# Kernel tuning notes

Hardware: AMD Instinct MI355X
Metric: run time of the kernel (lower is better)

The kernel has to match this reference:

```python
import jax, jax.numpy as jnp
import numpy as np

B, S, E, H = 2, 2048, 1024, 16
HD = E // H


def setup_inputs() -> dict:
    key = jax.random.key(0)
    ks = jax.random.split(key, 5)
    scale = 1.0 / np.sqrt(E)
    return {
        "x": jax.random.normal(ks[0], (B, S, E), dtype=jnp.float32),
        "Wq": jax.random.normal(ks[1], (H, HD, E), dtype=jnp.float32) * scale,
        "Wk": jax.random.normal(ks[2], (H, HD, E), dtype=jnp.float32) * scale,
        "Wv": jax.random.normal(ks[3], (H, HD, E), dtype=jnp.float32) * scale,
        "Wo": jax.random.normal(ks[4], (E, E), dtype=jnp.float32) * scale,
    }


def reference(x, Wq, Wk, Wv, Wo):
    # Batched per-head projections: torch Linear y = x @ W.T, W: [head_dim, E]
    q = jnp.einsum("bse,hde->bshd", x, Wq)  # [B,S,H,HD]
    k = jnp.einsum("bse,hde->bshd", x, Wk)
    v = jnp.einsum("bse,hde->bshd", x, Wv)
    # Scaled dot-product attention; original scales by sqrt(head_dim)
    scores = jnp.einsum("bqhd,bkhd->bhqk", q, k) / jnp.sqrt(jnp.float32(HD))
    attn = jax.nn.softmax(scores, axis=-1)  # [B,H,S,S]
    out_h = jnp.einsum("bhqk,bkhd->bqhd", attn, v)  # [B,S,H,HD]
    out_cat = out_h.reshape(x.shape[0], x.shape[1], -1)  # concat heads -> [B,S,E]
    return out_cat @ Wo.T
```

## Files before the change

### kernel.cpp

```cpp
#include <hip/hip_runtime.h>
#include <hip/hip_bf16.h>

typedef unsigned short u16;
typedef unsigned int u32;
typedef __attribute__((ext_vector_type(4))) float f32x4;
typedef __attribute__((ext_vector_type(16))) float f32x16;
typedef __attribute__((ext_vector_type(8))) short short8;
typedef __attribute__((ext_vector_type(8))) unsigned short u16x8;
typedef __attribute__((ext_vector_type(4))) unsigned short u16x4;
typedef __attribute__((ext_vector_type(4))) unsigned int u32x4;

#define BATCH 2
#define SEQ   2048
#define EMB   1024
#define NH    16
#define HD    64

__device__ inline u16 f2bf(float f) {
    unsigned u = __builtin_bit_cast(unsigned, f);
    unsigned r = u + 0x7FFFu + ((u >> 16) & 1u);
    return (u16)(r >> 16);
}

__device__ inline float fexp2(float x) {
    float r;
    asm("v_exp_f32 %0, %1" : "=v"(r) : "v"(x));
    return r;
}

__device__ inline void gload16(const void* g, void* l) {
    __builtin_amdgcn_global_load_lds(
        (const __attribute__((address_space(1))) unsigned int*)g,
        (__attribute__((address_space(3))) unsigned int*)l, 16, 0, 0);
}

__device__ inline short8 mk8(u32 a, u32 b, u32 c, u32 d) {
    u32x4 t; t[0] = a; t[1] = b; t[2] = c; t[3] = d;
    return __builtin_bit_cast(short8, t);
}

#define PACK_ST(st, w0,w1,w2,w3,w4,w5,w6,w7)                                   \
  {                                                                            \
    asm("v_cvt_pk_bf16_f32 %0, %1, %2" : "=v"(w0) : "v"(st[0]),  "v"(st[1]));  \
    asm("v_cvt_pk_bf16_f32 %0, %1, %2" : "=v"(w1) : "v"(st[2]),  "v"(st[3]));  \
    asm("v_cvt_pk_bf16_f32 %0, %1, %2" : "=v"(w2) : "v"(st[4]),  "v"(st[5]));  \
    asm("v_cvt_pk_bf16_f32 %0, %1, %2" : "=v"(w3) : "v"(st[6]),  "v"(st[7]));  \
    asm("v_permlane32_swap_b32 %0, %1" : "+v"(w0), "+v"(w2));                  \
    asm("v_permlane32_swap_b32 %0, %1" : "+v"(w1), "+v"(w3));                  \
    asm("v_cvt_pk_bf16_f32 %0, %1, %2" : "=v"(w4) : "v"(st[8]),  "v"(st[9]));  \
    asm("v_cvt_pk_bf16_f32 %0, %1, %2" : "=v"(w5) : "v"(st[10]), "v"(st[11])); \
    asm("v_cvt_pk_bf16_f32 %0, %1, %2" : "=v"(w6) : "v"(st[12]), "v"(st[13])); \
    asm("v_cvt_pk_bf16_f32 %0, %1, %2" : "=v"(w7) : "v"(st[14]), "v"(st[15])); \
    asm("v_permlane32_swap_b32 %0, %1" : "+v"(w4), "+v"(w6));                  \
    asm("v_permlane32_swap_b32 %0, %1" : "+v"(w5), "+v"(w7));                  \
  }

__global__ __launch_bounds__(256) void convert_all(
    const float* __restrict__ x,
    const float* __restrict__ Wq, const float* __restrict__ Wk, const float* __restrict__ Wv,
    const float* __restrict__ Wo,
    u16* __restrict__ Xb, u16* __restrict__ Wqkv, u16* __restrict__ Wob)
{
    const int bid = blockIdx.x;
    const float* src;
    u16* dst;
    if (bid < 3584) {
        const long gidx = (long)bid * 2048 + (long)threadIdx.x * 8;
        if (gidx < 4194304L) {
            src = x + gidx; dst = Xb + gidx;
        } else {
            const long r = gidx - 4194304L;
            const int w = (int)(r >> 20);
            const long off = r & 1048575L;
            src = (w == 0 ? Wq : w == 1 ? Wk : Wv) + off;
            dst = Wqkv + r;
        }
    } else {
        const long gidx = (long)(bid - 3584) * 2048 + (long)threadIdx.x * 8;
        src = Wo + gidx; dst = Wob + gidx;
    }
    f32x4 a = *(const f32x4*)src;
    f32x4 b = *(const f32x4*)(src + 4);
    u16x8 o;
    #pragma unroll
    for (int j = 0; j < 4; ++j) { o[j] = f2bf(a[j]); o[4 + j] = f2bf(b[j]); }
    *(u16x8*)dst = o;
}

__global__ __launch_bounds__(256) void convert_wo(
    const float* __restrict__ Wo, u16* __restrict__ Wob)
{
    const long gidx = (long)blockIdx.x * 2048 + (long)threadIdx.x * 8;
    f32x4 a = *(const f32x4*)(Wo + gidx);
    f32x4 b = *(const f32x4*)(Wo + gidx + 4);
    u16x8 o;
    #pragma unroll
    for (int j = 0; j < 4; ++j) { o[j] = f2bf(a[j]); o[4 + j] = f2bf(b[j]); }
    *(u16x8*)(Wob + gidx) = o;
}

__global__ __launch_bounds__(512, 2) void gemm256(
    const u16* __restrict__ A, const u16* __restrict__ Bb,
    u16* __restrict__ Qo, u16* __restrict__ Ko, u16* __restrict__ VTo)
{
    __shared__ u16 As[2][256 * 64];
    __shared__ u16 Bs[2][192 * 64];

    const int tid = threadIdx.x;
    const int lane = tid & 63;
    const int wid = tid >> 6;
    const int lr = lane & 15;
    const int lg = lane >> 4;
    const int wr = wid >> 2;
    const int wc = wid & 3;

    const int lin = blockIdx.y * 16 + blockIdx.x;
    const int swz = (lin & 7) * 32 + (lin >> 3);
    const int m0 = (swz & 15) * 256;
    const int n0 = (swz >> 4) * 192;

    const int grow = lane >> 3;
    const int schunk = ((lane & 7) ^ grow) << 4;

    auto issueTile = [&](int kt, int buf) {
        const int k0b = kt * 128;
        #pragma unroll
        for (int i = 0; i < 4; ++i) {
            const int row = i * 64 + wid * 8 + grow;
            gload16((const char*)A + (size_t)(m0 + row) * 2048 + k0b + schunk,
                    (char*)As[buf] + i * 8192 + wid * 1024);
        }
        #pragma unroll
        for (int i = 0; i < 3; ++i) {
            const int row = i * 64 + wid * 8 + grow;
            gload16((const char*)Bb + (size_t)(n0 + row) * 2048 + k0b + schunk,
                    (char*)Bs[buf] + i * 8192 + wid * 1024);
        }
    };

    issueTile(0, 0);
    issueTile(1, 1);

    f32x4 acc[8][3] = {};
    const int rsw = (lr & 7);

    for (int t = 0; t < 16; ++t) {
        if (t < 15) { asm volatile("s_waitcnt vmcnt(7)" ::: "memory"); }
        else        { asm volatile("s_waitcnt vmcnt(0)" ::: "memory"); }
        __builtin_amdgcn_sched_barrier(0);
        __builtin_amdgcn_s_barrier();
        __builtin_amdgcn_sched_barrier(0);

        const u16* Ac = As[t & 1];
        const u16* Bc = Bs[t & 1];

        short8 a[4][2], b[3][2];

        #pragma unroll
        for (int fi = 0; fi < 4; ++fi)
            #pragma unroll
            for (int ks = 0; ks < 2; ++ks)
                a[fi][ks] = *(const short8*)((const char*)Ac + (wr * 128 + fi * 16 + lr) * 128
                                             + (((ks * 4 + lg) ^ rsw) << 4));
        #pragma unroll
        for (int fj = 0; fj < 3; ++fj)
            #pragma unroll
            for (int ks = 0; ks < 2; ++ks)
                b[fj][ks] = *(const short8*)((const char*)Bc + (wc * 48 + fj * 16 + lr) * 128
                                             + (((ks * 4 + lg) ^ rsw) << 4));
        __builtin_amdgcn_s_setprio(1);
        #pragma unroll
        for (int fi = 0; fi < 4; ++fi)
            #pragma unroll
            for (int fj = 0; fj < 3; ++fj)
                #pragma unroll
                for (int ks = 0; ks < 2; ++ks)
                    acc[fi][fj] = __builtin_amdgcn_mfma_f32_16x16x32_bf16(a[fi][ks], b[fj][ks], acc[fi][fj], 0, 0, 0);
        __builtin_amdgcn_s_setprio(0);

        #pragma unroll
        for (int fi = 0; fi < 4; ++fi)
            #pragma unroll
            for (int ks = 0; ks < 2; ++ks)
                a[fi][ks] = *(const short8*)((const char*)Ac + (wr * 128 + (fi + 4) * 16 + lr) * 128
                                             + (((ks * 4 + lg) ^ rsw) << 4));
        __builtin_amdgcn_s_setprio(1);
        #pragma unroll
        for (int fi = 0; fi < 4; ++fi)
            #pragma unroll
            for (int fj = 0; fj < 3; ++fj)
                #pragma unroll
                for (int ks = 0; ks < 2; ++ks)
                    acc[fi + 4][fj] = __builtin_amdgcn_mfma_f32_16x16x32_bf16(a[fi][ks], b[fj][ks], acc[fi + 4][fj], 0, 0, 0);
        __builtin_amdgcn_s_setprio(0);

        __builtin_amdgcn_sched_barrier(0);
        __builtin_amdgcn_s_barrier();
        __builtin_amdgcn_sched_barrier(0);
        if (t + 2 < 16) issueTile(t + 2, t & 1);
    }

    const int mb = m0 + wr * 128;
    const int nb = n0 + wc * 48;
    #pragma unroll
    for (int fj = 0; fj < 3; ++fj) {
        const int nblk = nb + fj * 16;
        const int w = nblk >> 10;
        const float qs = (w == 0) ? 0.125f * 1.44269504f : 1.0f;
        const int nn = (nblk & 1023) + lr;
        const int h = nn >> 6, d = nn & 63;
        #pragma unroll
        for (int fi = 0; fi < 8; ++fi) {
            const int m = mb + fi * 16 + lg * 4;
            const int bb = m >> 11, s = m & 2047;
            const size_t bh = (size_t)(bb * NH + h);
            if (w == 2) {
                u16x4 v;
                #pragma unroll
                for (int i = 0; i < 4; ++i) v[i] = f2bf(acc[fi][fj][i]);
                *(u16x4*)&VTo[(bh * HD + d) * SEQ + s] = v;
            } else {
                u16* P = (w == 0) ? Qo : Ko;
                #pragma unroll
                for (int i = 0; i < 4; ++i)
                    P[(bh * SEQ + s + i) * HD + d] = f2bf(acc[fi][fj][i] * qs);
            }
        }
    }
}

__global__ __launch_bounds__(256) void gemm_out(
    const u16* __restrict__ A, const u16* __restrict__ Bb, float* __restrict__ Fo)
{
    __shared__ u16 As[2][128 * 64];
    __shared__ u16 Bs[2][128 * 64];

    const int tid = threadIdx.x;

    const int lin = blockIdx.y * 32 + blockIdx.x;
    const int swz = (lin & 7) * 32 + (lin >> 3);
    const int m0 = (swz & 31) * 128;
    const int n0 = (swz >> 5) * 128;

    const int lane = tid & 63;
    const int lr = lane & 15;
    const int lg = lane >> 4;
    const int wid = tid >> 6;
    const int wm = wid >> 1, wn = wid & 1;

    const int grow = lane >> 3;
    const int gcolb = ((lane & 7) ^ grow) << 4;
    const int rswz = (lr & 7);

    f32x4 acc[4][4] = {};

    auto issue = [&](int kt, int buf) {
        const int k0b = kt * 128;
        #pragma unroll
        for (int t = 0; t < 4; ++t) {
            const int row = (wid * 4 + t) * 8 + grow;
            gload16((const char*)A + (size_t)(m0 + row) * 2048 + k0b + gcolb,
                    (char*)As[buf] + (wid * 4 + t) * 1024);
            gload16((const char*)Bb + (size_t)(n0 + row) * 2048 + k0b + gcolb,
                    (char*)Bs[buf] + (wid * 4 + t) * 1024);
        }
    };

    issue(0, 0);
    issue(1, 1);

    for (int kt = 0; kt < 16; ++kt) {
        if (kt < 15) { asm volatile("s_waitcnt vmcnt(8)" ::: "memory"); }
        else         { asm volatile("s_waitcnt vmcnt(0)" ::: "memory"); }
        __builtin_amdgcn_sched_barrier(0);
        __builtin_amdgcn_s_barrier();
        __builtin_amdgcn_sched_barrier(0);

        const u16* Ac = As[kt & 1];
        const u16* Bc = Bs[kt & 1];
        #pragma unroll
        for (int kk = 0; kk < 2; ++kk) {
            short8 a[4], b[4];
            #pragma unroll
            for (int i = 0; i < 4; ++i)
                a[i] = *(const short8*)((const char*)Ac + (wm * 64 + i * 16 + lr) * 128
                                        + (((kk * 4 + lg) ^ rswz) << 4));
            #pragma unroll
            for (int i = 0; i < 4; ++i)
                b[i] = *(const short8*)((const char*)Bc + (wn * 64 + i * 16 + lr) * 128
                                        + (((kk * 4 + lg) ^ rswz) << 4));
            #pragma unroll
            for (int mi = 0; mi < 4; ++mi)
                #pragma unroll
                for (int ni = 0; ni < 4; ++ni)
                    acc[mi][ni] = __builtin_amdgcn_mfma_f32_16x16x32_bf16(a[mi], b[ni], acc[mi][ni], 0, 0, 0);
        }

        __builtin_amdgcn_sched_barrier(0);
        __builtin_amdgcn_s_barrier();
        __builtin_amdgcn_sched_barrier(0);
        if (kt + 2 < 16) issue(kt + 2, kt & 1);
    }

    const int mb = m0 + wm * 64;
    const int nb = n0 + wn * 64;
    #pragma unroll
    for (int mi = 0; mi < 4; ++mi)
        #pragma unroll
        for (int ni = 0; ni < 4; ++ni) {
            const int m = mb + mi * 16 + lg * 4;
            const int n = nb + ni * 16 + lr;
            #pragma unroll
            for (int i = 0; i < 4; ++i)
                Fo[(size_t)(m + i) * EMB + n] = acc[mi][ni][i];
        }
}

__global__ __launch_bounds__(256) void attn_fwd(
    const u16* __restrict__ Q, const u16* __restrict__ K,
    const u16* __restrict__ VT, u16* __restrict__ Cat)
{
    __shared__ u16 Ks[3][64 * 64];
    __shared__ u16 Vs[3][64 * 64];

    const int tid = threadIdx.x;
    const int lane = tid & 63;
    const int wid = tid >> 6;
    const int lq = lane & 31;
    const int hi = lane >> 5;

    const int lin = blockIdx.y * 16 + blockIdx.x;
    const int swz = (lin & 7) * 64 + (lin >> 3);
    const int qt = swz & 15;
    const int bh = swz >> 4;
    const int b = bh >> 4, h = bh & 15;

    const u16* Qg = Q + ((size_t)bh * SEQ + qt * 128 + wid * 32 + lq) * HD;
    short8 qf[4];
    #pragma unroll
    for (int ks = 0; ks < 4; ++ks)
        qf[ks] = *(const short8*)((const char*)Qg + ks * 32 + hi * 16);

    float lsum = 0.f;
    f32x16 ot0 = {}, ot1 = {};

    const u16* Kg = K + (size_t)bh * SEQ * HD;
    const u16* Vg = VT + (size_t)bh * HD * SEQ;

    const int srow = lane >> 3;
    const int schunk = ((lane & 7) ^ srow) << 4;

    auto issueKV = [&](int nt) {
        const int kv0 = nt * 64;
        const int slot = nt % 3;
        #pragma unroll
        for (int i = 0; i < 2; ++i) {
            const int krow = i * 32 + wid * 8 + srow;
            gload16((const char*)Kg + (size_t)(kv0 + krow) * 128 + schunk,
                    (char*)Ks[slot] + i * 4096 + wid * 1024);
            gload16((const char*)Vg + (size_t)krow * (SEQ * 2) + kv0 * 2 + schunk,
                    (char*)Vs[slot] + i * 4096 + wid * 1024);
        }
    };

    const int rsw = (lq & 7);

    auto tile2 = [&](const u16* KbufA, const u16* VbufA,
                     const u16* KbufB, const u16* VbufB) {
        f32x16 sA0 = {}, sA1 = {}, sB0 = {}, sB1 = {};
        #pragma unroll
        for (int ks = 0; ks < 4; ++ks) {
            const int co = ((ks * 2 + hi) ^ rsw) << 4;
            const short8 kA0 = *(const short8*)((const char*)KbufA + lq * 128 + co);
            const short8 kA1 = *(const short8*)((const char*)KbufA + (32 + lq) * 128 + co);
            const short8 kB0 = *(const short8*)((const char*)KbufB + lq * 128 + co);
            const short8 kB1 = *(const short8*)((const char*)KbufB + (32 + lq) * 128 + co);
            sA0 = __builtin_amdgcn_mfma_f32_32x32x16_bf16(kA0, qf[ks], sA0, 0, 0, 0);
            sA1 = __builtin_amdgcn_mfma_f32_32x32x16_bf16(kA1, qf[ks], sA1, 0, 0, 0);
            sB0 = __builtin_amdgcn_mfma_f32_32x32x16_bf16(kB0, qf[ks], sB0, 0, 0, 0);
            sB1 = __builtin_amdgcn_mfma_f32_32x32x16_bf16(kB1, qf[ks], sB1, 0, 0, 0);
        }

        #pragma unroll
        for (int i = 0; i < 16; ++i) {
            sA0[i] = fexp2(sA0[i]);
            sA1[i] = fexp2(sA1[i]);
            sB0[i] = fexp2(sB0[i]);
            sB1[i] = fexp2(sB1[i]);
        }
        float t0 = 0.f, t1 = 0.f, t2 = 0.f, t3 = 0.f;
        #pragma unroll
        for (int i = 0; i < 16; i += 4) {
            t0 += sA0[i]     + sA1[i]     + sB0[i]     + sB1[i];
            t1 += sA0[i + 1] + sA1[i + 1] + sB0[i + 1] + sB1[i + 1];
            t2 += sA0[i + 2] + sA1[i + 2] + sB0[i + 2] + sB1[i + 2];
            t3 += sA0[i + 3] + sA1[i + 3] + sB0[i + 3] + sB1[i + 3];
        }
        lsum += (t0 + t1) + (t2 + t3);

        u32 a0, a1, a2, a3, a4, a5, a6, a7;
        u32 c0, c1, c2, c3, c4, c5, c6, c7;
        PACK_ST(sA0, a0, a1, a2, a3, a4, a5, a6, a7);
        PACK_ST(sA1, c0, c1, c2, c3, c4, c5, c6, c7);
        const short8 pA0 = mk8(a0, a1, a2, a3);
        const short8 pA1 = mk8(a4, a5, a6, a7);
        const short8 pA2 = mk8(c0, c1, c2, c3);
        const short8 pA3 = mk8(c4, c5, c6, c7);
        u32 d0, d1, d2, d3, d4, d5, d6, d7;
        u32 e0, e1, e2, e3, e4, e5, e6, e7;
        PACK_ST(sB0, d0, d1, d2, d3, d4, d5, d6, d7);
        PACK_ST(sB1, e0, e1, e2, e3, e4, e5, e6, e7);
        const short8 pB0 = mk8(d0, d1, d2, d3);
        const short8 pB1 = mk8(d4, d5, d6, d7);
        const short8 pB2 = mk8(e0, e1, e2, e3);
        const short8 pB3 = mk8(e4, e5, e6, e7);

        #pragma unroll
        for (int ks = 0; ks < 4; ++ks) {
            const short8 pf = (ks == 0) ? pA0 : (ks == 1) ? pA1 : (ks == 2) ? pA2 : pA3;
            const int co = ((ks * 2 + hi) ^ rsw) << 4;
            const short8 vf0 = *(const short8*)((const char*)VbufA + lq * 128 + co);
            const short8 vf1 = *(const short8*)((const char*)VbufA + (32 + lq) * 128 + co);
            ot0 = __builtin_amdgcn_mfma_f32_32x32x16_bf16(vf0, pf, ot0, 0, 0, 0);
            ot1 = __builtin_amdgcn_mfma_f32_32x32x16_bf16(vf1, pf, ot1, 0, 0, 0);
        }
        #pragma unroll
        for (int ks = 0; ks < 4; ++ks) {
            const short8 pf = (ks == 0) ? pB0 : (ks == 1) ? pB1 : (ks == 2) ? pB2 : pB3;
            const int co = ((ks * 2 + hi) ^ rsw) << 4;
            const short8 vf0 = *(const short8*)((const char*)VbufB + lq * 128 + co);
            const short8 vf1 = *(const short8*)((const char*)VbufB + (32 + lq) * 128 + co);
            ot0 = __builtin_amdgcn_mfma_f32_32x32x16_bf16(vf0, pf, ot0, 0, 0, 0);
            ot1 = __builtin_amdgcn_mfma_f32_32x32x16_bf16(vf1, pf, ot1, 0, 0, 0);
        }
    };

    issueKV(0); issueKV(1); issueKV(2);

    for (int p = 0; p < 16; ++p) {
        if (p < 15) { asm volatile("s_waitcnt vmcnt(4)" ::: "memory"); }
        else        { asm volatile("s_waitcnt vmcnt(0)" ::: "memory"); }
        __builtin_amdgcn_sched_barrier(0);
        __builtin_amdgcn_s_barrier();
        __builtin_amdgcn_sched_barrier(0);

        const int s0 = (2 * p) % 3;
        const int s1 = (2 * p + 1) % 3;
        tile2(Ks[s0], Vs[s0], Ks[s1], Vs[s1]);

        __builtin_amdgcn_sched_barrier(0);
        __builtin_amdgcn_s_barrier();
        __builtin_amdgcn_sched_barrier(0);
        const int t3 = 2 * p + 3;
        if (t3 < 32)     issueKV(t3);
        if (t3 + 1 < 32) issueKV(t3 + 1);
    }

    const float l = lsum + __shfl_xor(lsum, 32);
    const float invl = 1.f / l;
    const int qrow = qt * 128 + wid * 32 + lq;
    u16* ob = Cat + ((size_t)b * SEQ + qrow) * EMB + h * HD;
    #pragma unroll
    for (int g = 0; g < 4; ++g) {
        u16x4 o0, o1;
        #pragma unroll
        for (int i = 0; i < 4; ++i) {
            o0[i] = f2bf(ot0[g * 4 + i] * invl);
            o1[i] = f2bf(ot1[g * 4 + i] * invl);
        }
        *(u16x4*)&ob[g * 8 + hi * 4] = o0;
        *(u16x4*)&ob[32 + g * 8 + hi * 4] = o1;
    }
}

extern "C" void kernel_launch(void* const* d_in, const int* in_sizes, int n_in,
                              void* d_out, int out_size, void* d_ws, size_t ws_size,
                              hipStream_t stream) {
    const float* x  = (const float*)d_in[0];
    const float* Wq = (const float*)d_in[1];
    const float* Wk = (const float*)d_in[2];
    const float* Wv = (const float*)d_in[3];
    const float* Wo = (const float*)d_in[4];
    float* out = (float*)d_out;

    u16* Xb   = (u16*)d_out;
    u16* Wqkv = (u16*)d_out + (size_t)4 * 1048576;

    char* ws = (char*)d_ws;
    u16* Qb  = (u16*)(ws);
    u16* Kb  = (u16*)(ws + (size_t)8  * 1048576);
    u16* VTb = (u16*)(ws + (size_t)16 * 1048576);
    u16* Cat = (u16*)(ws + (size_t)24 * 1048576);

    const bool bigws = ws_size >= (size_t)34 * 1048576;
    u16* Wob = bigws ? (u16*)(ws + (size_t)32 * 1048576) : Qb;

    convert_all<<<bigws ? 4096 : 3584, 256, 0, stream>>>(x, Wq, Wk, Wv, Wo,
                                                         Xb, Wqkv, Wob);

    dim3 g1(16, 16);
    gemm256<<<g1, 512, 0, stream>>>(Xb, Wqkv, Qb, Kb, VTb);

    dim3 g2(SEQ / 128, BATCH * NH);
    attn_fwd<<<g2, 256, 0, stream>>>(Qb, Kb, VTb, Cat);

    if (!bigws) convert_wo<<<512, 256, 0, stream>>>(Wo, Wob);
    dim3 g3(4096 / 128, 1024 / 128);
    gemm_out<<<g3, 256, 0, stream>>>(Cat, Wob, out);
}
```

Baseline: 114.1 us.

## Split attention KV range across two blocks and combine partial outputs

Adds a split-KV attention path. Each query tile is processed by two blocks, each covering half the keys, doubling the grid from 512 to 1024 blocks to improve occupancy and CU utilisation. Unnormalized fp32 partial outputs and row sums are written to workspace, and a separate combine kernel sums and normalizes them into bf16. The split is safe without max tracking because the code uses no running max. It costs extra fp32 global traffic (about 34 MB) and an extra launch, and it only runs when the workspace is at least 69 MB. The tile body is turned into a macro so both kernels share it.

```diff
diff --git a/kernel.cpp b/kernel.cpp
--- a/kernel.cpp
+++ b/kernel.cpp
@@ -316,6 +316,71 @@
         }
 }
 
+#define ATTN_TILE2_BODY(KbufA, VbufA, KbufB, VbufB)                            \
+  {                                                                            \
+    f32x16 sA0 = {}, sA1 = {}, sB0 = {}, sB1 = {};                             \
+    _Pragma("unroll")                                                          \
+    for (int ks = 0; ks < 4; ++ks) {                                           \
+        const int co = ((ks * 2 + hi) ^ rsw) << 4;                             \
+        const short8 kA0 = *(const short8*)((const char*)(KbufA) + lq * 128 + co);      \
+        const short8 kA1 = *(const short8*)((const char*)(KbufA) + (32 + lq) * 128 + co);\
+        const short8 kB0 = *(const short8*)((const char*)(KbufB) + lq * 128 + co);      \
+        const short8 kB1 = *(const short8*)((const char*)(KbufB) + (32 + lq) * 128 + co);\
+        sA0 = __builtin_amdgcn_mfma_f32_32x32x16_bf16(kA0, qf[ks], sA0, 0, 0, 0);       \
+        sA1 = __builtin_amdgcn_mfma_f32_32x32x16_bf16(kA1, qf[ks], sA1, 0, 0, 0);       \
+        sB0 = __builtin_amdgcn_mfma_f32_32x32x16_bf16(kB0, qf[ks], sB0, 0, 0, 0);       \
+        sB1 = __builtin_amdgcn_mfma_f32_32x32x16_bf16(kB1, qf[ks], sB1, 0, 0, 0);       \
+    }                                                                          \
+    _Pragma("unroll")                                                          \
+    for (int i = 0; i < 16; ++i) {                                             \
+        sA0[i] = fexp2(sA0[i]); sA1[i] = fexp2(sA1[i]);                        \
+        sB0[i] = fexp2(sB0[i]); sB1[i] = fexp2(sB1[i]);                        \
+    }                                                                          \
+    float t0 = 0.f, t1 = 0.f, t2 = 0.f, t3 = 0.f;                              \
+    _Pragma("unroll")                                                          \
+    for (int i = 0; i < 16; i += 4) {                                          \
+        t0 += sA0[i]     + sA1[i]     + sB0[i]     + sB1[i];                   \
+        t1 += sA0[i + 1] + sA1[i + 1] + sB0[i + 1] + sB1[i + 1];               \
+        t2 += sA0[i + 2] + sA1[i + 2] + sB0[i + 2] + sB1[i + 2];               \
+        t3 += sA0[i + 3] + sA1[i + 3] + sB0[i + 3] + sB1[i + 3];               \
+    }                                                                          \
+    lsum += (t0 + t1) + (t2 + t3);                                             \
+    u32 a0, a1, a2, a3, a4, a5, a6, a7;                                        \
+    u32 c0, c1, c2, c3, c4, c5, c6, c7;                                        \
+    PACK_ST(sA0, a0, a1, a2, a3, a4, a5, a6, a7);                              \
+    PACK_ST(sA1, c0, c1, c2, c3, c4, c5, c6, c7);                              \
+    const short8 pA0 = mk8(a0, a1, a2, a3);                                    \
+    const short8 pA1 = mk8(a4, a5, a6, a7);                                    \
+    const short8 pA2 = mk8(c0, c1, c2, c3);                                    \
+    const short8 pA3 = mk8(c4, c5, c6, c7);                                    \
+    u32 d0, d1, d2, d3, d4, d5, d6, d7;                                        \
+    u32 e0, e1, e2, e3, e4, e5, e6, e7;                                        \
+    PACK_ST(sB0, d0, d1, d2, d3, d4, d5, d6, d7);                              \
+    PACK_ST(sB1, e0, e1, e2, e3, e4, e5, e6, e7);                              \
+    const short8 pB0 = mk8(d0, d1, d2, d3);                                    \
+    const short8 pB1 = mk8(d4, d5, d6, d7);                                    \
+    const short8 pB2 = mk8(e0, e1, e2, e3);                                    \
+    const short8 pB3 = mk8(e4, e5, e6, e7);                                    \
+    _Pragma("unroll")                                                          \
+    for (int ks = 0; ks < 4; ++ks) {                                           \
+        const short8 pf = (ks == 0) ? pA0 : (ks == 1) ? pA1 : (ks == 2) ? pA2 : pA3;    \
+        const int co = ((ks * 2 + hi) ^ rsw) << 4;                             \
+        const short8 vf0 = *(const short8*)((const char*)(VbufA) + lq * 128 + co);      \
+        const short8 vf1 = *(const short8*)((const char*)(VbufA) + (32 + lq) * 128 + co);\
+        ot0 = __builtin_amdgcn_mfma_f32_32x32x16_bf16(vf0, pf, ot0, 0, 0, 0);  \
+        ot1 = __builtin_amdgcn_mfma_f32_32x32x16_bf16(vf1, pf, ot1, 0, 0, 0);  \
+    }                                                                          \
+    _Pragma("unroll")                                                          \
+    for (int ks = 0; ks < 4; ++ks) {                                           \
+        const short8 pf = (ks == 0) ? pB0 : (ks == 1) ? pB1 : (ks == 2) ? pB2 : pB3;    \
+        const int co = ((ks * 2 + hi) ^ rsw) << 4;                             \
+        const short8 vf0 = *(const short8*)((const char*)(VbufB) + lq * 128 + co);      \
+        const short8 vf1 = *(const short8*)((const char*)(VbufB) + (32 + lq) * 128 + co);\
+        ot0 = __builtin_amdgcn_mfma_f32_32x32x16_bf16(vf0, pf, ot0, 0, 0, 0);  \
+        ot1 = __builtin_amdgcn_mfma_f32_32x32x16_bf16(vf1, pf, ot1, 0, 0, 0);  \
+    }                                                                          \
+  }
+
 __global__ __launch_bounds__(256) void attn_fwd(
     const u16* __restrict__ Q, const u16* __restrict__ K,
     const u16* __restrict__ VT, u16* __restrict__ Cat)
@@ -365,76 +430,6 @@
 
     const int rsw = (lq & 7);
 
-    auto tile2 = [&](const u16* KbufA, const u16* VbufA,
-                     const u16* KbufB, const u16* VbufB) {
-        f32x16 sA0 = {}, sA1 = {}, sB0 = {}, sB1 = {};
-        #pragma unroll
-        for (int ks = 0; ks < 4; ++ks) {
-            const int co = ((ks * 2 + hi) ^ rsw) << 4;
-            const short8 kA0 = *(const short8*)((const char*)KbufA + lq * 128 + co);
-            const short8 kA1 = *(const short8*)((const char*)KbufA + (32 + lq) * 128 + co);
-            const short8 kB0 = *(const short8*)((const char*)KbufB + lq * 128 + co);
-            const short8 kB1 = *(const short8*)((const char*)KbufB + (32 + lq) * 128 + co);
-            sA0 = __builtin_amdgcn_mfma_f32_32x32x16_bf16(kA0, qf[ks], sA0, 0, 0, 0);
-            sA1 = __builtin_amdgcn_mfma_f32_32x32x16_bf16(kA1, qf[ks], sA1, 0, 0, 0);
-            sB0 = __builtin_amdgcn_mfma_f32_32x32x16_bf16(kB0, qf[ks], sB0, 0, 0, 0);
-            sB1 = __builtin_amdgcn_mfma_f32_32x32x16_bf16(kB1, qf[ks], sB1, 0, 0, 0);
-        }
-
-        #pragma unroll
-        for (int i = 0; i < 16; ++i) {
-            sA0[i] = fexp2(sA0[i]);
-            sA1[i] = fexp2(sA1[i]);
-            sB0[i] = fexp2(sB0[i]);
-            sB1[i] = fexp2(sB1[i]);
-        }
-        float t0 = 0.f, t1 = 0.f, t2 = 0.f, t3 = 0.f;
-        #pragma unroll
-        for (int i = 0; i < 16; i += 4) {
-            t0 += sA0[i]     + sA1[i]     + sB0[i]     + sB1[i];
-            t1 += sA0[i + 1] + sA1[i + 1] + sB0[i + 1] + sB1[i + 1];
-            t2 += sA0[i + 2] + sA1[i + 2] + sB0[i + 2] + sB1[i + 2];
-            t3 += sA0[i + 3] + sA1[i + 3] + sB0[i + 3] + sB1[i + 3];
-        }
-        lsum += (t0 + t1) + (t2 + t3);
-
-        u32 a0, a1, a2, a3, a4, a5, a6, a7;
-        u32 c0, c1, c2, c3, c4, c5, c6, c7;
-        PACK_ST(sA0, a0, a1, a2, a3, a4, a5, a6, a7);
-        PACK_ST(sA1, c0, c1, c2, c3, c4, c5, c6, c7);
-        const short8 pA0 = mk8(a0, a1, a2, a3);
-        const short8 pA1 = mk8(a4, a5, a6, a7);
-        const short8 pA2 = mk8(c0, c1, c2, c3);
-        const short8 pA3 = mk8(c4, c5, c6, c7);
-        u32 d0, d1, d2, d3, d4, d5, d6, d7;
-        u32 e0, e1, e2, e3, e4, e5, e6, e7;
-        PACK_ST(sB0, d0, d1, d2, d3, d4, d5, d6, d7);
-        PACK_ST(sB1, e0, e1, e2, e3, e4, e5, e6, e7);
-        const short8 pB0 = mk8(d0, d1, d2, d3);
-        const short8 pB1 = mk8(d4, d5, d6, d7);
-        const short8 pB2 = mk8(e0, e1, e2, e3);
-        const short8 pB3 = mk8(e4, e5, e6, e7);
-
-        #pragma unroll
-        for (int ks = 0; ks < 4; ++ks) {
-            const short8 pf = (ks == 0) ? pA0 : (ks == 1) ? pA1 : (ks == 2) ? pA2 : pA3;
-            const int co = ((ks * 2 + hi) ^ rsw) << 4;
-            const short8 vf0 = *(const short8*)((const char*)VbufA + lq * 128 + co);
-            const short8 vf1 = *(const short8*)((const char*)VbufA + (32 + lq) * 128 + co);
-            ot0 = __builtin_amdgcn_mfma_f32_32x32x16_bf16(vf0, pf, ot0, 0, 0, 0);
-            ot1 = __builtin_amdgcn_mfma_f32_32x32x16_bf16(vf1, pf, ot1, 0, 0, 0);
-        }
-        #pragma unroll
-        for (int ks = 0; ks < 4; ++ks) {
-            const short8 pf = (ks == 0) ? pB0 : (ks == 1) ? pB1 : (ks == 2) ? pB2 : pB3;
-            const int co = ((ks * 2 + hi) ^ rsw) << 4;
-            const short8 vf0 = *(const short8*)((const char*)VbufB + lq * 128 + co);
-            const short8 vf1 = *(const short8*)((const char*)VbufB + (32 + lq) * 128 + co);
-            ot0 = __builtin_amdgcn_mfma_f32_32x32x16_bf16(vf0, pf, ot0, 0, 0, 0);
-            ot1 = __builtin_amdgcn_mfma_f32_32x32x16_bf16(vf1, pf, ot1, 0, 0, 0);
-        }
-    };
-
     issueKV(0); issueKV(1); issueKV(2);
 
     for (int p = 0; p < 16; ++p) {
@@ -446,7 +441,7 @@
 
         const int s0 = (2 * p) % 3;
         const int s1 = (2 * p + 1) % 3;
-        tile2(Ks[s0], Vs[s0], Ks[s1], Vs[s1]);
+        ATTN_TILE2_BODY(Ks[s0], Vs[s0], Ks[s1], Vs[s1]);
 
         __builtin_amdgcn_sched_barrier(0);
         __builtin_amdgcn_s_barrier();
@@ -471,6 +466,115 @@
         *(u16x4*)&ob[g * 8 + hi * 4] = o0;
         *(u16x4*)&ob[32 + g * 8 + hi * 4] = o1;
     }
+}
+
+__global__ __launch_bounds__(256) void attn_split(
+    const u16* __restrict__ Q, const u16* __restrict__ K,
+    const u16* __restrict__ VT, float* __restrict__ Op, float* __restrict__ lp)
+{
+    __shared__ u16 Ks[3][64 * 64];
+    __shared__ u16 Vs[3][64 * 64];
+
+    const int tid = threadIdx.x;
+    const int lane = tid & 63;
+    const int wid = tid >> 6;
+    const int lq = lane & 31;
+    const int hi = lane >> 5;
+
+    const int lin = blockIdx.x;
+    const int swz = (lin & 7) * 128 + (lin >> 3);
+    const int half = swz & 1;
+    const int qt = (swz >> 1) & 15;
+    const int bh = swz >> 5;
+
+    const u16* Qg = Q + ((size_t)bh * SEQ + qt * 128 + wid * 32 + lq) * HD;
+    short8 qf[4];
+    #pragma unroll
+    for (int ks = 0; ks < 4; ++ks)
+        qf[ks] = *(const short8*)((const char*)Qg + ks * 32 + hi * 16);
+
+    float lsum = 0.f;
+    f32x16 ot0 = {}, ot1 = {};
+
+    const u16* Kg = K + (size_t)bh * SEQ * HD;
+    const u16* Vg = VT + (size_t)bh * HD * SEQ;
+
+    const int srow = lane >> 3;
+    const int schunk = ((lane & 7) ^ srow) << 4;
+
+    auto issueKV = [&](int nt) {
+        const int kv0 = (half * 16 + nt) * 64;
+        const int slot = nt % 3;
+        #pragma unroll
+        for (int i = 0; i < 2; ++i) {
+            const int krow = i * 32 + wid * 8 + srow;
+            gload16((const char*)Kg + (size_t)(kv0 + krow) * 128 + schunk,
+                    (char*)Ks[slot] + i * 4096 + wid * 1024);
+            gload16((const char*)Vg + (size_t)krow * (SEQ * 2) + kv0 * 2 + schunk,
+                    (char*)Vs[slot] + i * 4096 + wid * 1024);
+        }
+    };
+
+    const int rsw = (lq & 7);
+
+    issueKV(0); issueKV(1); issueKV(2);
+
+    for (int p = 0; p < 8; ++p) {
+        if (p < 7) { asm volatile("s_waitcnt vmcnt(4)" ::: "memory"); }
+        else       { asm volatile("s_waitcnt vmcnt(0)" ::: "memory"); }
+        __builtin_amdgcn_sched_barrier(0);
+        __builtin_amdgcn_s_barrier();
+        __builtin_amdgcn_sched_barrier(0);
+
+        const int s0 = (2 * p) % 3;
+        const int s1 = (2 * p + 1) % 3;
+        ATTN_TILE2_BODY(Ks[s0], Vs[s0], Ks[s1], Vs[s1]);
+
+        __builtin_amdgcn_sched_barrier(0);
+        __builtin_amdgcn_s_barrier();
+        __builtin_amdgcn_sched_barrier(0);
+        const int t3 = 2 * p + 3;
+        if (t3 < 16)     issueKV(t3);
+        if (t3 + 1 < 16) issueKV(t3 + 1);
+    }
+
+    const float lfull = lsum + __shfl_xor(lsum, 32);
+    const int gq = bh * SEQ + qt * 128 + wid * 32 + lq;
+    float* ob = Op + (size_t)half * (65536ull * 64) + (size_t)gq * 64;
+    #pragma unroll
+    for (int g = 0; g < 4; ++g) {
+        f32x4 o0, o1;
+        #pragma unroll
+        for (int i = 0; i < 4; ++i) { o0[i] = ot0[g * 4 + i]; o1[i] = ot1[g * 4 + i]; }
+        *(f32x4*)&ob[g * 8 + hi * 4] = o0;
+        *(f32x4*)&ob[32 + g * 8 + hi * 4] = o1;
+    }
+    if (hi == 0) lp[half * 65536 + gq] = lfull;
+}
+
+__global__ __launch_bounds__(256) void combine_halves(
+    const float* __restrict__ Op, const float* __restrict__ lp,
+    u16* __restrict__ Cat)
+{
+    const int idx8 = blockIdx.x * 256 + threadIdx.x;
+    const int gq = idx8 >> 3;
+    const int dc = idx8 & 7;
+    const float inv = 1.f / (lp[gq] + lp[65536 + gq]);
+    const float* p0 = Op + (size_t)gq * 64 + dc * 8;
+    const float* p1 = p0 + 65536ull * 64;
+    const f32x4 a0 = *(const f32x4*)p0;
+    const f32x4 a1 = *(const f32x4*)(p0 + 4);
+    const f32x4 b0 = *(const f32x4*)p1;
+    const f32x4 b1 = *(const f32x4*)(p1 + 4);
+    u16x8 o;
+    #pragma unroll
+    for (int j = 0; j < 4; ++j) {
+        o[j]     = f2bf((a0[j] + b0[j]) * inv);
+        o[4 + j] = f2bf((a1[j] + b1[j]) * inv);
+    }
+    const int bh = gq >> 11, s = gq & 2047;
+    const int b = bh >> 4, h = bh & 15;
+    *(u16x8*)&Cat[(size_t)b * (SEQ * EMB) + (size_t)s * EMB + h * HD + dc * 8] = o;
 }
 
 extern "C" void kernel_launch(void* const* d_in, const int* in_sizes, int n_in,
@@ -493,7 +597,10 @@
     u16* Cat = (u16*)(ws + (size_t)24 * 1048576);
 
     const bool bigws = ws_size >= (size_t)34 * 1048576;
+    const bool split = ws_size >= (size_t)69 * 1048576;
     u16* Wob = bigws ? (u16*)(ws + (size_t)32 * 1048576) : Qb;
+    float* Op = (float*)(ws + (size_t)34 * 1048576);
+    float* lp = (float*)(ws + (size_t)68 * 1048576);
 
     convert_all<<<bigws ? 4096 : 3584, 256, 0, stream>>>(x, Wq, Wk, Wv, Wo,
                                                          Xb, Wqkv, Wob);
@@ -501,8 +608,13 @@
     dim3 g1(16, 16);
     gemm256<<<g1, 512, 0, stream>>>(Xb, Wqkv, Qb, Kb, VTb);
 
-    dim3 g2(SEQ / 128, BATCH * NH);
-    attn_fwd<<<g2, 256, 0, stream>>>(Qb, Kb, VTb, Cat);
+    if (split) {
+        attn_split<<<1024, 256, 0, stream>>>(Qb, Kb, VTb, Op, lp);
+        combine_halves<<<2048, 256, 0, stream>>>(Op, lp, Cat);
+    } else {
+        dim3 g2(SEQ / 128, BATCH * NH);
+        attn_fwd<<<g2, 256, 0, stream>>>(Qb, Kb, VTb, Cat);
+    }
 
     if (!bigws) convert_wo<<<512, 256, 0, stream>>>(Wo, Wob);
     dim3 g3(4096 / 128, 1024 / 128);
```

Result: slower. 121.8 us (+6.8%).
